# Kernel tuning notes

Measured on AMD Instinct MI355X. Metric: run time of the kernel, lower is better.

Reference implementation:

```python
import math
import jax, jax.numpy as jnp
import numpy as np

D_MODEL = 1024
NUM_HEADS = 16
D_HEAD = D_MODEL // NUM_HEADS  # 64
K_S = 32  # sparse top-k keys kept per query
B, N = 2, 2048


def setup_inputs() -> dict:
    key = jax.random.key(0)
    ks = jax.random.split(key, 9)
    s = 1.0 / math.sqrt(D_MODEL)
    return {
        "x": jax.random.normal(ks[0], (B, N, D_MODEL), dtype=jnp.float32),
        "Wq": jax.random.normal(ks[1], (D_MODEL, D_MODEL), dtype=jnp.float32) * s,
        "bq": jnp.zeros((D_MODEL,), dtype=jnp.float32),
        "Wk": jax.random.normal(ks[2], (D_MODEL, D_MODEL), dtype=jnp.float32) * s,
        "bk": jnp.zeros((D_MODEL,), dtype=jnp.float32),
        "Wv": jax.random.normal(ks[3], (D_MODEL, D_MODEL), dtype=jnp.float32) * s,
        "bv": jnp.zeros((D_MODEL,), dtype=jnp.float32),
        "Wo": jax.random.normal(ks[4], (D_MODEL, D_MODEL), dtype=jnp.float32) * s,
        "bo": jnp.zeros((D_MODEL,), dtype=jnp.float32),
    }


def _attn(x, Wq, bq, Wk, bk, Wv, bv, Wo, bo):
    b, n, _ = x.shape
    # projections (torch Linear: y = x W^T + b)
    q = (x @ Wq.T + bq).reshape(b, n, NUM_HEADS, D_HEAD).transpose(0, 2, 1, 3)
    k = (x @ Wk.T + bk).reshape(b, n, NUM_HEADS, D_HEAD).transpose(0, 2, 1, 3)
    v = (x @ Wv.T + bv).reshape(b, n, NUM_HEADS, D_HEAD).transpose(0, 2, 1, 3)
    # full scores [b, H, n, n]
    scores = jnp.einsum("bhqd,bhkd->bhqk", q, k) / math.sqrt(D_HEAD)
    # causal mask (triu above diagonal -> -inf)
    causal = jnp.triu(jnp.ones((n, n), dtype=bool), k=1)
    neg_inf = jnp.array(-jnp.inf, dtype=scores.dtype)
    scores = jnp.where(causal, neg_inf, scores)
    # sparse top-k: keep only K_S largest scores per query row
    vals, idx = jax.lax.top_k(scores, K_S)
    masked = jnp.full_like(scores, -jnp.inf)
    masked = jnp.put_along_axis(masked, idx, vals, axis=-1, inplace=False)
    attn = jax.nn.softmax(masked, axis=-1)  # dropout p=0.0 -> identity
    out = jnp.einsum("bhqk,bhkd->bhqd", attn, v)
    out = out.transpose(0, 2, 1, 3).reshape(b, n, D_MODEL)
    y = out @ Wo.T + bo
    return y, attn.mean(axis=1)


def reference(x, Wq, bq, Wk, bk, Wv, bv, Wo, bo):
    return _attn(x, Wq, bq, Wk, bk, Wv, bv, Wo, bo)
```

## Files before the change

kernel.cpp:

```cpp
#include <hip/hip_runtime.h>
#include <hip/hip_bf16.h>
#include <math.h>

#define BATCH   2
#define NTOK    2048
#define DMODEL  1024
#define HEADS   16
#define DHEAD   64
#define KSEL    32
#define MROWS   (BATCH * NTOK)
#define NBLK8   (NTOK / 8)

typedef short     bf16x8 __attribute__((ext_vector_type(8)));
typedef float     f32x4  __attribute__((ext_vector_type(4)));
typedef unsigned short ushort_t;
typedef unsigned long long u64;

#define GLOAD_LDS16(g, l) \
    __builtin_amdgcn_global_load_lds((const __attribute__((address_space(1))) void*)(g), \
                                     (__attribute__((address_space(3))) void*)(l), 16, 0, 0)

__device__ __forceinline__ ushort_t f2bf(float f) {
    unsigned u = __float_as_uint(f);
    unsigned r = (u + 0x7FFFu + ((u >> 16) & 1u)) >> 16;
    return (ushort_t)r;
}
__device__ __forceinline__ float bf2f(ushort_t h) {
    return __uint_as_float(((unsigned)h) << 16);
}

__global__ __launch_bounds__(256) void conv_split(const float* __restrict__ in,
                                                  ushort_t* __restrict__ hi,
                                                  ushort_t* __restrict__ lo, int n)
{
    const int i = (blockIdx.x * 256 + threadIdx.x) * 4;
    if (i + 3 < n) {
        const float4 v = *(const float4*)(in + i);
        ushort4 ph, pl;
        ph.x = f2bf(v.x); pl.x = f2bf(v.x - bf2f(ph.x));
        ph.y = f2bf(v.y); pl.y = f2bf(v.y - bf2f(ph.y));
        ph.z = f2bf(v.z); pl.z = f2bf(v.z - bf2f(ph.z));
        ph.w = f2bf(v.w); pl.w = f2bf(v.w - bf2f(ph.w));
        *(ushort4*)(hi + i) = ph;
        *(ushort4*)(lo + i) = pl;
    }
}

__global__ __launch_bounds__(256) void zero_fill(float* __restrict__ p, int n4)
{
    const int i = blockIdx.x * 256 + threadIdx.x;
    if (i < n4) ((float4*)p)[i] = (float4){0.f, 0.f, 0.f, 0.f};
}

__device__ __forceinline__ unsigned mono_key(float f) {
    const unsigned u = __float_as_uint(f);
    return (u ^ (unsigned)(((int)u >> 31) | 0x80000000)) + 1u;
}
__device__ __forceinline__ float unmono(unsigned m) {
    const unsigned u = m - 1u;
    return __uint_as_float(u ^ (unsigned)(((int)(~u) >> 31) | 0x80000000));
}

__global__ __launch_bounds__(256) void gemm_split_mfma(const ushort_t* __restrict__ Ahi,
                                                       const ushort_t* __restrict__ Alo,
                                                       const ushort_t* __restrict__ Bhi,
                                                       const ushort_t* __restrict__ Blo,
                                                       const float* __restrict__ bias,
                                                       float* __restrict__ out,
                                                       ushort_t* __restrict__ oh,
                                                       ushort_t* __restrict__ om,
                                                       ushort_t* __restrict__ ol,
                                                       int mode)
{
    __shared__ ushort_t AbufH[128 * 32];
    __shared__ ushort_t AbufL[128 * 32];
    __shared__ ushort_t BbufH[64 * 32];
    __shared__ ushort_t BbufL[64 * 32];

    const int tid  = threadIdx.x;
    const int wave = tid >> 6;
    const int lane = tid & 63;
    const int m0 = blockIdx.x * 128;
    const int n0 = blockIdx.y * 64;

    f32x4 acc[2][4];
#pragma unroll
    for (int i = 0; i < 2; ++i)
#pragma unroll
        for (int j = 0; j < 4; ++j) acc[i][j] = (f32x4){0.f, 0.f, 0.f, 0.f};

    const int ar0 = tid >> 2;
    const int ar1 = 64 + (tid >> 2);
    const int ak  = (tid & 3) << 3;
    const int br  = tid >> 2;

    const int fr = lane & 15;
    const int fk = (lane >> 4) << 3;

    for (int k0 = 0; k0 < DMODEL; k0 += 32) {
        __syncthreads();
        const size_t aoff0 = (size_t)(m0 + ar0) * DMODEL + k0 + ak;
        const size_t aoff1 = (size_t)(m0 + ar1) * DMODEL + k0 + ak;
        const size_t boff  = (size_t)(n0 + br) * DMODEL + k0 + ak;
        GLOAD_LDS16(Ahi + aoff0, AbufH + (size_t)tid * 8);
        GLOAD_LDS16(Ahi + aoff1, AbufH + (size_t)(256 + tid) * 8);
        GLOAD_LDS16(Alo + aoff0, AbufL + (size_t)tid * 8);
        GLOAD_LDS16(Alo + aoff1, AbufL + (size_t)(256 + tid) * 8);
        GLOAD_LDS16(Bhi + boff, BbufH + (size_t)tid * 8);
        GLOAD_LDS16(Blo + boff, BbufL + (size_t)tid * 8);
        __syncthreads();

        bf16x8 afh[2], afl[2], bfh[4], bfl[4];
#pragma unroll
        for (int mi = 0; mi < 2; ++mi) {
            const int ro = (wave * 32 + mi * 16 + fr) * 32 + fk;
            afh[mi] = *(const bf16x8*)(AbufH + ro);
            afl[mi] = *(const bf16x8*)(AbufL + ro);
        }
#pragma unroll
        for (int ni = 0; ni < 4; ++ni) {
            const int ro = (ni * 16 + fr) * 32 + fk;
            bfh[ni] = *(const bf16x8*)(BbufH + ro);
            bfl[ni] = *(const bf16x8*)(BbufL + ro);
        }

#pragma unroll
        for (int mi = 0; mi < 2; ++mi)
#pragma unroll
            for (int ni = 0; ni < 4; ++ni) {
                acc[mi][ni] = __builtin_amdgcn_mfma_f32_16x16x32_bf16(afh[mi], bfl[ni], acc[mi][ni], 0, 0, 0);
                acc[mi][ni] = __builtin_amdgcn_mfma_f32_16x16x32_bf16(afl[mi], bfh[ni], acc[mi][ni], 0, 0, 0);
                acc[mi][ni] = __builtin_amdgcn_mfma_f32_16x16x32_bf16(afh[mi], bfh[ni], acc[mi][ni], 0, 0, 0);
            }
    }

#pragma unroll
    for (int ni = 0; ni < 4; ++ni) {
        const int o = n0 + ni * 16 + (lane & 15);
        const float bv = bias[o];
#pragma unroll
        for (int mi = 0; mi < 2; ++mi) {
#pragma unroll
            for (int reg = 0; reg < 4; ++reg) {
                const int m = m0 + wave * 32 + mi * 16 + ((lane >> 4) << 2) + reg;
                const float v = acc[mi][ni][reg] + bv;
                if (mode == 0) {
                    out[(size_t)m * DMODEL + o] = v;
                } else {
                    const int bb = m >> 11;
                    const int n  = m & 2047;
                    const int hd = o >> 6;
                    const int d  = o & 63;
                    const size_t off = (((size_t)(bb * HEADS + hd)) * NTOK + n) * DHEAD + d;
                    if (mode == 1) {
                        out[off] = v;
                    } else {
                        const ushort_t h1 = f2bf(v);
                        const float r1 = v - bf2f(h1);
                        const ushort_t m1 = f2bf(r1);
                        const ushort_t l1 = f2bf(r1 - bf2f(m1));
                        oh[off] = h1; om[off] = m1; ol[off] = l1;
                    }
                }
            }
        }
    }
}

__global__ __launch_bounds__(256) void score_mfma(const ushort_t* __restrict__ Qh,
                                                  const ushort_t* __restrict__ Qm,
                                                  const ushort_t* __restrict__ Ql,
                                                  const ushort_t* __restrict__ Kh,
                                                  const ushort_t* __restrict__ Km,
                                                  const ushort_t* __restrict__ Kl,
                                                  unsigned* __restrict__ S,
                                                  unsigned* __restrict__ Smax,
                                                  int q0, int QC)
{
    const int kt = blockIdx.x;
    const int qt = blockIdx.y;
    const int bh = blockIdx.z;
    const int qbase = q0 + qt * 128;
    if (kt * 64 > qbase + 127) return;

    __shared__ ushort_t QhB[128 * 32], QmB[128 * 32], QlB[128 * 32];
    __shared__ ushort_t KhB[64 * 32],  KmB[64 * 32],  KlB[64 * 32];

    const int tid  = threadIdx.x;
    const int wave = tid >> 6;
    const int lane = tid & 63;

    const size_t qgbase = ((size_t)bh * NTOK + qbase) * DHEAD;
    const size_t kgbase = ((size_t)bh * NTOK + kt * 64) * DHEAD;

    f32x4 acc[2][4];
#pragma unroll
    for (int i = 0; i < 2; ++i)
#pragma unroll
        for (int j = 0; j < 4; ++j) acc[i][j] = (f32x4){0.f, 0.f, 0.f, 0.f};

#pragma unroll
    for (int kit = 0; kit < 2; ++kit) {
        const int koff = kit * 32;
        __syncthreads();
#pragma unroll
        for (int i = 0; i < 2; ++i) {
            const int c = i * 256 + tid;
            const int row = c >> 2;
            const int pos = (c & 3) ^ ((row >> 1) & 3);
            const size_t g = qgbase + (size_t)row * DHEAD + koff + pos * 8;
            GLOAD_LDS16(Qh + g, QhB + (size_t)c * 8);
            GLOAD_LDS16(Qm + g, QmB + (size_t)c * 8);
            GLOAD_LDS16(Ql + g, QlB + (size_t)c * 8);
        }
        {
            const int c = tid;
            const int row = c >> 2;
            const int pos = (c & 3) ^ ((row >> 1) & 3);
            const size_t g = kgbase + (size_t)row * DHEAD + koff + pos * 8;
            GLOAD_LDS16(Kh + g, KhB + (size_t)c * 8);
            GLOAD_LDS16(Km + g, KmB + (size_t)c * 8);
            GLOAD_LDS16(Kl + g, KlB + (size_t)c * 8);
        }
        __syncthreads();

        const int k8 = lane >> 4;

        bf16x8 qhf[2], qmf[2], qlf[2];
#pragma unroll
        for (int mi = 0; mi < 2; ++mi) {
            const int r = wave * 32 + mi * 16 + (lane & 15);
            const int ch = r * 4 + (k8 ^ ((r >> 1) & 3));
            qhf[mi] = *(const bf16x8*)(QhB + (size_t)ch * 8);
            qmf[mi] = *(const bf16x8*)(QmB + (size_t)ch * 8);
            qlf[mi] = *(const bf16x8*)(QlB + (size_t)ch * 8);
        }
        bf16x8 khf[4], kmf[4], klf[4];
#pragma unroll
        for (int ni = 0; ni < 4; ++ni) {
            const int r = ni * 16 + (lane & 15);
            const int ch = r * 4 + (k8 ^ ((r >> 1) & 3));
            khf[ni] = *(const bf16x8*)(KhB + (size_t)ch * 8);
            kmf[ni] = *(const bf16x8*)(KmB + (size_t)ch * 8);
            klf[ni] = *(const bf16x8*)(KlB + (size_t)ch * 8);
        }

#pragma unroll
        for (int mi = 0; mi < 2; ++mi)
#pragma unroll
            for (int ni = 0; ni < 4; ++ni) {
                acc[mi][ni] = __builtin_amdgcn_mfma_f32_16x16x32_bf16(qhf[mi], klf[ni], acc[mi][ni], 0, 0, 0);
                acc[mi][ni] = __builtin_amdgcn_mfma_f32_16x16x32_bf16(qlf[mi], khf[ni], acc[mi][ni], 0, 0, 0);
                acc[mi][ni] = __builtin_amdgcn_mfma_f32_16x16x32_bf16(qmf[mi], kmf[ni], acc[mi][ni], 0, 0, 0);
                acc[mi][ni] = __builtin_amdgcn_mfma_f32_16x16x32_bf16(qhf[mi], kmf[ni], acc[mi][ni], 0, 0, 0);
                acc[mi][ni] = __builtin_amdgcn_mfma_f32_16x16x32_bf16(qmf[mi], khf[ni], acc[mi][ni], 0, 0, 0);
                acc[mi][ni] = __builtin_amdgcn_mfma_f32_16x16x32_bf16(qhf[mi], khf[ni], acc[mi][ni], 0, 0, 0);
            }
    }

#pragma unroll
    for (int ni = 0; ni < 4; ++ni) {
        const int col = kt * 64 + ni * 16 + (lane & 15);
#pragma unroll
        for (int mi = 0; mi < 2; ++mi) {
#pragma unroll
            for (int reg = 0; reg < 4; ++reg) {
                const int mrow = wave * 32 + mi * 16 + ((lane >> 4) << 2) + reg;
                const int qlrow = qt * 128 + mrow;
                const int qglob = qbase + mrow;
                const unsigned mk = mono_key(acc[mi][ni][reg] * 0.125f);
                S[((size_t)bh * QC + qlrow) * NTOK + col] = mk;
                unsigned cm = (col <= qglob) ? mk : 0u;
                {
                    unsigned o;
                    o = __shfl_xor(cm, 1, 64); cm = (o > cm) ? o : cm;
                    o = __shfl_xor(cm, 2, 64); cm = (o > cm) ? o : cm;
                    o = __shfl_xor(cm, 4, 64); cm = (o > cm) ? o : cm;
                }
                if ((lane & 7) == 0) {
                    const int gblk = kt * 8 + ni * 2 + ((lane >> 3) & 1);
                    Smax[((size_t)bh * QC + qlrow) * NBLK8 + gblk] = cm;
                }
            }
        }
    }
}

__global__ __launch_bounds__(256) void select_v6(const unsigned* __restrict__ S,
                                                 const unsigned* __restrict__ Smax,
                                                 const float* __restrict__ V,
                                                 float* __restrict__ ctx,
                                                 float* __restrict__ attn,
                                                 int q0, int QC)
{
    __shared__ int   sBlkAll[4][KSEL];
    __shared__ int   sIdxAll[4][KSEL];
    __shared__ float sEAll[4][KSEL];

    const int lane = threadIdx.x & 63;
    const int wave = threadIdx.x >> 6;
    const int ql = blockIdx.x;
    const int b  = blockIdx.y >> 2;
    const int hg = blockIdx.y & 3;
    const int h  = hg * 4 + wave;
    const int q  = q0 + ql;
    const int L  = q + 1;
    const int nsel = (L < KSEL) ? L : KSEL;
    const int nb = (L + 7) >> 3;

    const size_t bhx = (size_t)(b * HEADS + h);
    const unsigned* Srow = S + (bhx * QC + ql) * NTOK;
    const unsigned* Mrow = Smax + (bhx * QC + ql) * NBLK8;
    const float* Vb   = V + bhx * NTOK * DHEAD;
    float* ctxRow  = ctx + (((size_t)(b * NTOK + q)) * HEADS + h) * DHEAD;
    float* attnRow = attn + ((size_t)(b * NTOK + q)) * NTOK;
    int*   sBlk = sBlkAll[wave];
    int*   sIdx = sIdxAll[wave];
    float* sE   = sEAll[wave];

    const uint4 bm4 = *(const uint4*)(Mrow + lane * 4);
    unsigned bmax[4] = {bm4.x, bm4.y, bm4.z, bm4.w};
#pragma unroll
    for (int s = 0; s < 4; ++s)
        if (lane * 4 + s >= nb) bmax[s] = 0u;

    unsigned gmax = bmax[0];
    gmax = (bmax[1] > gmax) ? bmax[1] : gmax;
    gmax = (bmax[2] > gmax) ? bmax[2] : gmax;
    gmax = (bmax[3] > gmax) ? bmax[3] : gmax;
#pragma unroll
    for (int d = 1; d < 64; d <<= 1) {
        const unsigned o = __shfl_xor(gmax, d, 64);
        gmax = (o > gmax) ? o : gmax;
    }
    const float vmax = unmono(gmax);

    unsigned selb = 0u;
    unsigned blkLo = 1u;
    int nselb;
    if (nb <= KSEL) {
        nselb = nb;
#pragma unroll
        for (int s = 0; s < 4; ++s)
            if (lane * 4 + s < nb) selb |= 1u << s;
    } else {
        nselb = KSEL;
        unsigned lo = 1u, hi = gmax >> 16;
        while (lo < hi) {
            const unsigned mid = lo + ((hi - lo + 1u) >> 1);
            const unsigned midk = mid << 16;
            int cnt = 0;
#pragma unroll
            for (int s = 0; s < 4; ++s)
                cnt += __popcll(__ballot(bmax[s] >= midk));
            if (cnt >= KSEL) lo = mid; else hi = mid - 1u;
        }
        blkLo = lo;
        const unsigned Tkb = lo << 16;
        const unsigned Gkb = Tkb | 0xFFFFu;
        int cge = 0, cgt = 0;
#pragma unroll
        for (int s = 0; s < 4; ++s) {
            cge += __popcll(__ballot(bmax[s] >= Tkb));
            cgt += __popcll(__ballot(bmax[s] > Gkb));
        }
        if (cge == KSEL) {
#pragma unroll
            for (int s = 0; s < 4; ++s)
                selb |= (bmax[s] >= Tkb) ? (1u << s) : 0u;
        } else {
            unsigned bmb = 0u;
#pragma unroll
            for (int s = 0; s < 4; ++s) {
                selb |= (bmax[s] > Gkb) ? (1u << s) : 0u;
                bmb  |= (bmax[s] >= Tkb && bmax[s] <= Gkb) ? (1u << s) : 0u;
            }
            int k_tie = KSEL - cgt;
            while (k_tie > 0) {
                u64 best = 0;
                unsigned bmm = bmb;
                while (bmm) {
                    const int s = __builtin_ctz(bmm);
                    bmm &= bmm - 1u;
                    const unsigned gblk = (unsigned)(lane * 4 + s);
                    const u64 k = ((u64)bmax[s] << 32) | (unsigned)~gblk;
                    if (k > best) best = k;
                }
                u64 bb = best;
#pragma unroll
                for (int d = 1; d < 64; d <<= 1) {
                    const u64 o = __shfl_xor(bb, d, 64);
                    bb = (o > bb) ? o : bb;
                }
                const unsigned gblk = ~(unsigned)bb;
                if (lane == (int)(gblk >> 2)) {
                    const unsigned bit = 1u << (gblk & 3u);
                    selb |= bit;
                    bmb &= ~bit;
                }
                --k_tie;
            }
        }
    }

    {
        const int cb = __popc(selb);
        int pfxb = cb;
#pragma unroll
        for (int d = 1; d < 64; d <<= 1) {
            const int t = __shfl_up(pfxb, d, 64);
            if (lane >= d) pfxb += t;
        }
        pfxb -= cb;
        unsigned mskb = selb;
        int posb = pfxb;
        while (mskb) {
            const int s = __builtin_ctz(mskb);
            mskb &= mskb - 1u;
            sBlk[posb++] = lane * 4 + s;
        }
    }
    __asm volatile("s_waitcnt lgkmcnt(0)" ::: "memory");

    const int NC = nselb * 8;
    unsigned km[4];
    int idx[4];
#pragma unroll
    for (int c = 0; c < 4; ++c) {
        const int t = c * 64 + lane;
        unsigned m = 0u;
        int j = 0;
        if (t < NC) {
            const int blk = sBlk[t >> 3];
            j = blk * 8 + (t & 7);
            if (j < L) m = Srow[j];
        }
        km[c] = m;
        idx[c] = j;
    }

    unsigned lo = blkLo, hi = gmax >> 16;
    while (lo < hi) {
        const unsigned mid = lo + ((hi - lo + 1u) >> 1);
        const unsigned midk = mid << 16;
        int cnt = 0;
#pragma unroll
        for (int c = 0; c < 4; ++c)
            cnt += __popcll(__ballot(km[c] >= midk));
        if (cnt >= nsel) lo = mid; else hi = mid - 1u;
    }
    const unsigned Tk = lo << 16;
    const unsigned Gk = Tk | 0xFFFFu;

    int cnt_ge = 0, cnt_gt = 0;
#pragma unroll
    for (int c = 0; c < 4; ++c) {
        cnt_ge += __popcll(__ballot(km[c] >= Tk));
        cnt_gt += __popcll(__ballot(km[c] > Gk));
    }

    unsigned selmask = 0u;
    if (cnt_ge == nsel) {
#pragma unroll
        for (int c = 0; c < 4; ++c)
            selmask |= (km[c] >= Tk) ? (1u << c) : 0u;
    } else {
        unsigned bmask = 0u;
#pragma unroll
        for (int c = 0; c < 4; ++c) {
            selmask |= (km[c] > Gk) ? (1u << c) : 0u;
            bmask   |= (km[c] >= Tk && km[c] <= Gk) ? (1u << c) : 0u;
        }
        int k_tie = nsel - cnt_gt;
        while (k_tie > 0) {
            u64 best = 0;
            unsigned bmm = bmask;
            while (bmm) {
                const int c = __builtin_ctz(bmm);
                bmm &= bmm - 1u;
                const int t = c * 64 + lane;
                const u64 k = ((u64)km[c] << 32) |
                              ((u64)(0xFFFFu ^ (unsigned)idx[c]) << 16) | (u64)t;
                if (k > best) best = k;
            }
            u64 bb = best;
#pragma unroll
            for (int d = 1; d < 64; d <<= 1) {
                const u64 o = __shfl_xor(bb, d, 64);
                bb = (o > bb) ? o : bb;
            }
            const unsigned tt = (unsigned)bb & 0xFFFFu;
            if (lane == (int)(tt & 63u)) {
                const unsigned bit = 1u << (tt >> 6);
                selmask |= bit;
                bmask &= ~bit;
            }
            --k_tie;
        }
    }

    const int csel = __popc(selmask);
    int pfx = csel;
#pragma unroll
    for (int d = 1; d < 64; d <<= 1) {
        const int t = __shfl_up(pfx, d, 64);
        if (lane >= d) pfx += t;
    }
    pfx -= csel;

    float esum = 0.f;
    unsigned msk = selmask;
    int pos = pfx;
    while (msk) {
        const int c = __builtin_ctz(msk);
        msk &= msk - 1u;
        const float e = __expf(unmono(km[c]) - vmax);
        esum += e;
        sIdx[pos] = idx[c];
        sE[pos] = e;
        ++pos;
    }

    float Z = esum;
#pragma unroll
    for (int d = 1; d < 64; d <<= 1) Z += __shfl_xor(Z, d, 64);
    const float rcpZ = 1.0f / Z;

    msk = selmask;
    pos = pfx;
    while (msk) {
        const int c = __builtin_ctz(msk);
        msk &= msk - 1u;
        const float w = sE[pos] * rcpZ;
        ++pos;
        atomicAdd(&attnRow[idx[c]], w * (1.0f / (float)HEADS));
    }

    float acc = 0.f;
    for (int i = 0; i < nsel; ++i) {
        const int id = sIdx[i];
        const float wi = sE[i] * rcpZ;
        acc += wi * Vb[(size_t)id * DHEAD + lane];
    }
    ctxRow[lane] = acc;
}

extern "C" void kernel_launch(void* const* d_in, const int* in_sizes, int n_in,
                              void* d_out, int out_size, void* d_ws, size_t ws_size,
                              hipStream_t stream) {
    const float* x  = (const float*)d_in[0];
    const float* Wq = (const float*)d_in[1];
    const float* bq = (const float*)d_in[2];
    const float* Wk = (const float*)d_in[3];
    const float* bk = (const float*)d_in[4];
    const float* Wv = (const float*)d_in[5];
    const float* bv = (const float*)d_in[6];
    const float* Wo = (const float*)d_in[7];
    const float* bo = (const float*)d_in[8];

    const size_t MB = 1ull << 20;
    char* wsb = (char*)d_ws;
    float*    Vws = (float*)(wsb + 0 * MB);
    float*    ctx = (float*)(wsb + 16 * MB);
    ushort_t* xhi = (ushort_t*)(wsb + 32 * MB);
    ushort_t* xlo = (ushort_t*)(wsb + 40 * MB);
    ushort_t* wqh = (ushort_t*)(wsb + 48 * MB);
    ushort_t* wql = (ushort_t*)(wsb + 50 * MB);
    ushort_t* wkh = (ushort_t*)(wsb + 52 * MB);
    ushort_t* wkl = (ushort_t*)(wsb + 54 * MB);
    ushort_t* wvh = (ushort_t*)(wsb + 56 * MB);
    ushort_t* wvl = (ushort_t*)(wsb + 58 * MB);
    ushort_t* woh = (ushort_t*)(wsb + 60 * MB);
    ushort_t* wol = (ushort_t*)(wsb + 62 * MB);
    ushort_t* Qh  = (ushort_t*)(wsb + 64 * MB);
    ushort_t* Qm  = (ushort_t*)(wsb + 72 * MB);
    ushort_t* Ql  = (ushort_t*)(wsb + 80 * MB);
    ushort_t* Kh  = (ushort_t*)(wsb + 88 * MB);
    ushort_t* Km  = (ushort_t*)(wsb + 96 * MB);
    ushort_t* Kl  = (ushort_t*)(wsb + 104 * MB);
    ushort_t* cxh = xhi;
    ushort_t* cxl = xlo;

    float* y    = (float*)d_out;
    float* attn = y + (size_t)BATCH * NTOK * DMODEL;

    const int NX = MROWS * DMODEL;
    const int NW = DMODEL * DMODEL;

    conv_split<<<NX / (256 * 4), 256, 0, stream>>>(x, xhi, xlo, NX);
    conv_split<<<NW / (256 * 4), 256, 0, stream>>>(Wq, wqh, wql, NW);
    conv_split<<<NW / (256 * 4), 256, 0, stream>>>(Wk, wkh, wkl, NW);
    conv_split<<<NW / (256 * 4), 256, 0, stream>>>(Wv, wvh, wvl, NW);
    conv_split<<<NW / (256 * 4), 256, 0, stream>>>(Wo, woh, wol, NW);

    dim3 ggrid(MROWS / 128, DMODEL / 64);
    gemm_split_mfma<<<ggrid, 256, 0, stream>>>(xhi, xlo, wqh, wql, bq, nullptr, Qh, Qm, Ql, 2);
    gemm_split_mfma<<<ggrid, 256, 0, stream>>>(xhi, xlo, wkh, wkl, bk, nullptr, Kh, Km, Kl, 2);
    gemm_split_mfma<<<ggrid, 256, 0, stream>>>(xhi, xlo, wvh, wvl, bv, Vws, nullptr, nullptr, nullptr, 1);

    const size_t base_bytes = 112 * MB;
    const size_t avail = (ws_size > base_bytes) ? ws_size - base_bytes : 0;
    int QC = 128;
    for (int cand = NTOK; cand >= 128; cand >>= 1) {
        const size_t need = (size_t)BATCH * HEADS * cand * (size_t)(NTOK + NBLK8) * sizeof(unsigned);
        if (need <= avail) { QC = cand; break; }
    }
    unsigned* Smax = (unsigned*)(wsb + base_bytes);
    unsigned* Sws  = (unsigned*)(wsb + base_bytes +
                                 (size_t)BATCH * HEADS * QC * NBLK8 * sizeof(unsigned));

    const int nattn4 = BATCH * NTOK * NTOK / 4;
    zero_fill<<<(nattn4 + 255) / 256, 256, 0, stream>>>(attn, nattn4);
    for (int q0 = 0; q0 < NTOK; q0 += QC) {
        dim3 sgrid((q0 + QC) >> 6, QC / 128, BATCH * HEADS);
        score_mfma<<<sgrid, 256, 0, stream>>>(Qh, Qm, Ql, Kh, Km, Kl, Sws, Smax, q0, QC);
        dim3 selgrid(QC, BATCH * 4);
        select_v6<<<selgrid, 256, 0, stream>>>(Sws, Smax, Vws, ctx, attn, q0, QC);
    }

    conv_split<<<NX / (256 * 4), 256, 0, stream>>>(ctx, cxh, cxl, NX);
    gemm_split_mfma<<<ggrid, 256, 0, stream>>>(cxh, cxl, woh, wol, bo, y, nullptr, nullptr, nullptr, 0);
}
```

Measured before the change: 602.5 us.

## Keep Q fragments in registers and stream 8 K tiles per score block

The score kernel now loads the 128-row Q tile once, keeps its three split-bf16 planes in registers, and loops over up to eight 64-key K tiles per block with double-buffered asynchronous LDS staging. Before, every key tile reloaded Q. The MFMA operands are swapped (K as A, Q as B), so each lane holds four consecutive key columns and writes them with a single uint4 store, which also cuts the shuffle reduction for block maxima to one step. Launch bounds request 3 blocks per CU. The trade-offs are higher register pressure and fewer blocks in the grid, which may leave the causal triangle's work unevenly spread across blocks.

Result: faster. 553.5 us (-8.1%).

```diff
diff --git a/kernel.cpp b/kernel.cpp
--- a/kernel.cpp
+++ b/kernel.cpp
@@ -10,6 +10,7 @@
 #define KSEL    32
 #define MROWS   (BATCH * NTOK)
 #define NBLK8   (NTOK / 8)
+#define TPW     8
 
 typedef short     bf16x8 __attribute__((ext_vector_type(8)));
 typedef float     f32x4  __attribute__((ext_vector_type(4)));
@@ -167,123 +168,170 @@
     }
 }
 
-__global__ __launch_bounds__(256) void score_mfma(const ushort_t* __restrict__ Qh,
-                                                  const ushort_t* __restrict__ Qm,
-                                                  const ushort_t* __restrict__ Ql,
-                                                  const ushort_t* __restrict__ Kh,
-                                                  const ushort_t* __restrict__ Km,
-                                                  const ushort_t* __restrict__ Kl,
-                                                  unsigned* __restrict__ S,
-                                                  unsigned* __restrict__ Smax,
-                                                  int q0, int QC)
+__global__ __launch_bounds__(256, 3) void score_mfma(const ushort_t* __restrict__ Qh,
+                                                     const ushort_t* __restrict__ Qm,
+                                                     const ushort_t* __restrict__ Ql,
+                                                     const ushort_t* __restrict__ Kh,
+                                                     const ushort_t* __restrict__ Km,
+                                                     const ushort_t* __restrict__ Kl,
+                                                     unsigned* __restrict__ S,
+                                                     unsigned* __restrict__ Smax,
+                                                     int q0, int QC)
 {
-    const int kt = blockIdx.x;
+    const int ks = blockIdx.x;
     const int qt = blockIdx.y;
     const int bh = blockIdx.z;
     const int qbase = q0 + qt * 128;
-    if (kt * 64 > qbase + 127) return;
-
-    __shared__ ushort_t QhB[128 * 32], QmB[128 * 32], QlB[128 * 32];
-    __shared__ ushort_t KhB[64 * 32],  KmB[64 * 32],  KlB[64 * 32];
+    const int ktmax = ((qbase + 127) >> 6) + 1;
+    const int kt0 = ks * TPW;
+    if (kt0 >= ktmax) return;
+    const int kt1 = (kt0 + TPW < ktmax) ? (kt0 + TPW) : ktmax;
+
+    __shared__ ushort_t smem[24576];
 
     const int tid  = threadIdx.x;
     const int wave = tid >> 6;
     const int lane = tid & 63;
+    const int l15  = lane & 15;
+    const int l4   = lane >> 4;
 
     const size_t qgbase = ((size_t)bh * NTOK + qbase) * DHEAD;
-    const size_t kgbase = ((size_t)bh * NTOK + kt * 64) * DHEAD;
-
-    f32x4 acc[2][4];
-#pragma unroll
-    for (int i = 0; i < 2; ++i)
-#pragma unroll
-        for (int j = 0; j < 4; ++j) acc[i][j] = (f32x4){0.f, 0.f, 0.f, 0.f};
-
-#pragma unroll
-    for (int kit = 0; kit < 2; ++kit) {
-        const int koff = kit * 32;
+
+    {
+        const ushort_t* Qp0 = Qh; const ushort_t* Qp1 = Qm; const ushort_t* Qp2 = Ql;
+#pragma unroll
+        for (int i = 0; i < 4; ++i) {
+            const int c = i * 256 + tid;
+            const int row = c >> 3;
+            const int g = (c & 7) ^ (row & 7);
+            const size_t goff = qgbase + (size_t)row * DHEAD + g * 8;
+            GLOAD_LDS16(Qp0 + goff, smem + 0 * 8192 + (size_t)c * 8);
+            GLOAD_LDS16(Qp1 + goff, smem + 1 * 8192 + (size_t)c * 8);
+            GLOAD_LDS16(Qp2 + goff, smem + 2 * 8192 + (size_t)c * 8);
+        }
+    }
+    __syncthreads();
+
+    bf16x8 qf[3][2][2];
+#pragma unroll
+    for (int p = 0; p < 3; ++p)
+#pragma unroll
+        for (int j = 0; j < 2; ++j) {
+            const int r = wave * 32 + j * 16 + l15;
+#pragma unroll
+            for (int h = 0; h < 2; ++h) {
+                const int slot = (h * 4 + l4) ^ (r & 7);
+                qf[p][j][h] = *(const bf16x8*)(smem + p * 8192 + (size_t)(r * 8 + slot) * 8);
+            }
+        }
+    __syncthreads();
+
+#define STAGE_K(bufsel, ktv) do {                                              \
+        const size_t kg_ = ((size_t)bh * NTOK + (ktv) * 64) * DHEAD;           \
+        _Pragma("unroll")                                                      \
+        for (int i_ = 0; i_ < 2; ++i_) {                                       \
+            const int c_ = i_ * 256 + tid;                                     \
+            const int row_ = c_ >> 3;                                          \
+            const int g_ = (c_ & 7) ^ (row_ & 7);                              \
+            const size_t goff_ = kg_ + (size_t)row_ * DHEAD + g_ * 8;          \
+            ushort_t* dst_ = smem + (bufsel) * 12288 + (size_t)c_ * 8;         \
+            GLOAD_LDS16(Kh + goff_, dst_ + 0 * 4096);                          \
+            GLOAD_LDS16(Km + goff_, dst_ + 1 * 4096);                          \
+            GLOAD_LDS16(Kl + goff_, dst_ + 2 * 4096);                          \
+        }                                                                      \
+    } while (0)
+
+    STAGE_K(0, kt0);
+    int cur = 0;
+
+    const size_t srowQ = (size_t)bh * QC;
+
+    for (int kt = kt0; kt < kt1; ++kt) {
         __syncthreads();
-#pragma unroll
-        for (int i = 0; i < 2; ++i) {
-            const int c = i * 256 + tid;
-            const int row = c >> 2;
-            const int pos = (c & 3) ^ ((row >> 1) & 3);
-            const size_t g = qgbase + (size_t)row * DHEAD + koff + pos * 8;
-            GLOAD_LDS16(Qh + g, QhB + (size_t)c * 8);
-            GLOAD_LDS16(Qm + g, QmB + (size_t)c * 8);
-            GLOAD_LDS16(Ql + g, QlB + (size_t)c * 8);
-        }
-        {
-            const int c = tid;
-            const int row = c >> 2;
-            const int pos = (c & 3) ^ ((row >> 1) & 3);
-            const size_t g = kgbase + (size_t)row * DHEAD + koff + pos * 8;
-            GLOAD_LDS16(Kh + g, KhB + (size_t)c * 8);
-            GLOAD_LDS16(Km + g, KmB + (size_t)c * 8);
-            GLOAD_LDS16(Kl + g, KlB + (size_t)c * 8);
-        }
-        __syncthreads();
-
-        const int k8 = lane >> 4;
-
-        bf16x8 qhf[2], qmf[2], qlf[2];
-#pragma unroll
-        for (int mi = 0; mi < 2; ++mi) {
-            const int r = wave * 32 + mi * 16 + (lane & 15);
-            const int ch = r * 4 + (k8 ^ ((r >> 1) & 3));
-            qhf[mi] = *(const bf16x8*)(QhB + (size_t)ch * 8);
-            qmf[mi] = *(const bf16x8*)(QmB + (size_t)ch * 8);
-            qlf[mi] = *(const bf16x8*)(QlB + (size_t)ch * 8);
-        }
-        bf16x8 khf[4], kmf[4], klf[4];
-#pragma unroll
-        for (int ni = 0; ni < 4; ++ni) {
-            const int r = ni * 16 + (lane & 15);
-            const int ch = r * 4 + (k8 ^ ((r >> 1) & 3));
-            khf[ni] = *(const bf16x8*)(KhB + (size_t)ch * 8);
-            kmf[ni] = *(const bf16x8*)(KmB + (size_t)ch * 8);
-            klf[ni] = *(const bf16x8*)(KlB + (size_t)ch * 8);
-        }
-
-#pragma unroll
-        for (int mi = 0; mi < 2; ++mi)
-#pragma unroll
-            for (int ni = 0; ni < 4; ++ni) {
-                acc[mi][ni] = __builtin_amdgcn_mfma_f32_16x16x32_bf16(qhf[mi], klf[ni], acc[mi][ni], 0, 0, 0);
-                acc[mi][ni] = __builtin_amdgcn_mfma_f32_16x16x32_bf16(qlf[mi], khf[ni], acc[mi][ni], 0, 0, 0);
-                acc[mi][ni] = __builtin_amdgcn_mfma_f32_16x16x32_bf16(qmf[mi], kmf[ni], acc[mi][ni], 0, 0, 0);
-                acc[mi][ni] = __builtin_amdgcn_mfma_f32_16x16x32_bf16(qhf[mi], kmf[ni], acc[mi][ni], 0, 0, 0);
-                acc[mi][ni] = __builtin_amdgcn_mfma_f32_16x16x32_bf16(qmf[mi], khf[ni], acc[mi][ni], 0, 0, 0);
-                acc[mi][ni] = __builtin_amdgcn_mfma_f32_16x16x32_bf16(qhf[mi], khf[ni], acc[mi][ni], 0, 0, 0);
-            }
-    }
-
-#pragma unroll
-    for (int ni = 0; ni < 4; ++ni) {
-        const int col = kt * 64 + ni * 16 + (lane & 15);
-#pragma unroll
-        for (int mi = 0; mi < 2; ++mi) {
-#pragma unroll
-            for (int reg = 0; reg < 4; ++reg) {
-                const int mrow = wave * 32 + mi * 16 + ((lane >> 4) << 2) + reg;
-                const int qlrow = qt * 128 + mrow;
-                const int qglob = qbase + mrow;
-                const unsigned mk = mono_key(acc[mi][ni][reg] * 0.125f);
-                S[((size_t)bh * QC + qlrow) * NTOK + col] = mk;
-                unsigned cm = (col <= qglob) ? mk : 0u;
-                {
-                    unsigned o;
-                    o = __shfl_xor(cm, 1, 64); cm = (o > cm) ? o : cm;
-                    o = __shfl_xor(cm, 2, 64); cm = (o > cm) ? o : cm;
-                    o = __shfl_xor(cm, 4, 64); cm = (o > cm) ? o : cm;
+        if (kt + 1 < kt1) STAGE_K(cur ^ 1, kt + 1);
+
+        f32x4 acc[4][2];
+#pragma unroll
+        for (int m = 0; m < 4; ++m)
+#pragma unroll
+            for (int j = 0; j < 2; ++j) acc[m][j] = (f32x4){0.f, 0.f, 0.f, 0.f};
+
+        const ushort_t* kb = smem + cur * 12288;
+#pragma unroll
+        for (int h = 0; h < 2; ++h) {
+            bf16x8 kf[4];
+#pragma unroll
+            for (int m = 0; m < 4; ++m) {
+                const int r = m * 16 + l15;
+                const int slot = (h * 4 + l4) ^ (r & 7);
+                kf[m] = *(const bf16x8*)(kb + 0 * 4096 + (size_t)(r * 8 + slot) * 8);
+            }
+#pragma unroll
+            for (int m = 0; m < 4; ++m)
+#pragma unroll
+                for (int j = 0; j < 2; ++j) {
+                    acc[m][j] = __builtin_amdgcn_mfma_f32_16x16x32_bf16(kf[m], qf[2][j][h], acc[m][j], 0, 0, 0);
+                    acc[m][j] = __builtin_amdgcn_mfma_f32_16x16x32_bf16(kf[m], qf[1][j][h], acc[m][j], 0, 0, 0);
+                    acc[m][j] = __builtin_amdgcn_mfma_f32_16x16x32_bf16(kf[m], qf[0][j][h], acc[m][j], 0, 0, 0);
                 }
-                if ((lane & 7) == 0) {
-                    const int gblk = kt * 8 + ni * 2 + ((lane >> 3) & 1);
-                    Smax[((size_t)bh * QC + qlrow) * NBLK8 + gblk] = cm;
+#pragma unroll
+            for (int m = 0; m < 4; ++m) {
+                const int r = m * 16 + l15;
+                const int slot = (h * 4 + l4) ^ (r & 7);
+                kf[m] = *(const bf16x8*)(kb + 1 * 4096 + (size_t)(r * 8 + slot) * 8);
+            }
+#pragma unroll
+            for (int m = 0; m < 4; ++m)
+#pragma unroll
+                for (int j = 0; j < 2; ++j) {
+                    acc[m][j] = __builtin_amdgcn_mfma_f32_16x16x32_bf16(kf[m], qf[1][j][h], acc[m][j], 0, 0, 0);
+                    acc[m][j] = __builtin_amdgcn_mfma_f32_16x16x32_bf16(kf[m], qf[0][j][h], acc[m][j], 0, 0, 0);
                 }
-            }
-        }
-    }
+#pragma unroll
+            for (int m = 0; m < 4; ++m) {
+                const int r = m * 16 + l15;
+                const int slot = (h * 4 + l4) ^ (r & 7);
+                kf[m] = *(const bf16x8*)(kb + 2 * 4096 + (size_t)(r * 8 + slot) * 8);
+            }
+#pragma unroll
+            for (int m = 0; m < 4; ++m)
+#pragma unroll
+                for (int j = 0; j < 2; ++j)
+                    acc[m][j] = __builtin_amdgcn_mfma_f32_16x16x32_bf16(kf[m], qf[0][j][h], acc[m][j], 0, 0, 0);
+        }
+
+#pragma unroll
+        for (int j = 0; j < 2; ++j) {
+            const int qrow  = wave * 32 + j * 16 + l15;
+            const int qlrow = qt * 128 + qrow;
+            const int qglob = qbase + qrow;
+            const size_t srow = (srowQ + qlrow) * NTOK;
+            const size_t mrow = (srowQ + qlrow) * NBLK8;
+#pragma unroll
+            for (int m = 0; m < 4; ++m) {
+                const int kcol0 = kt * 64 + m * 16 + (l4 << 2);
+                uint4 kv;
+                kv.x = mono_key(acc[m][j][0] * 0.125f);
+                kv.y = mono_key(acc[m][j][1] * 0.125f);
+                kv.z = mono_key(acc[m][j][2] * 0.125f);
+                kv.w = mono_key(acc[m][j][3] * 0.125f);
+                *(uint4*)(S + srow + kcol0) = kv;
+                unsigned cm = (kcol0     <= qglob) ? kv.x : 0u;
+                unsigned t;
+                t = (kcol0 + 1 <= qglob) ? kv.y : 0u; cm = (t > cm) ? t : cm;
+                t = (kcol0 + 2 <= qglob) ? kv.z : 0u; cm = (t > cm) ? t : cm;
+                t = (kcol0 + 3 <= qglob) ? kv.w : 0u; cm = (t > cm) ? t : cm;
+                const unsigned o = __shfl_xor(cm, 16, 64);
+                cm = (o > cm) ? o : cm;
+                if ((lane & 16) == 0) {
+                    const int gblk = kt * 8 + m * 2 + (lane >> 5);
+                    Smax[mrow + gblk] = cm;
+                }
+            }
+        }
+        cur ^= 1;
+    }
+#undef STAGE_K
 }
 
 __global__ __launch_bounds__(256) void select_v6(const unsigned* __restrict__ S,
@@ -612,7 +660,8 @@
     const int nattn4 = BATCH * NTOK * NTOK / 4;
     zero_fill<<<(nattn4 + 255) / 256, 256, 0, stream>>>(attn, nattn4);
     for (int q0 = 0; q0 < NTOK; q0 += QC) {
-        dim3 sgrid((q0 + QC) >> 6, QC / 128, BATCH * HEADS);
+        const int ktm = (q0 + QC) >> 6;
+        dim3 sgrid((ktm + TPW - 1) / TPW, QC / 128, BATCH * HEADS);
         score_mfma<<<sgrid, 256, 0, stream>>>(Qh, Qm, Ql, Kh, Km, Kl, Sws, Smax, q0, QC);
         dim3 selgrid(QC, BATCH * 4);
         select_v6<<<selgrid, 256, 0, stream>>>(Sws, Smax, Vws, ctx, attn, q0, QC);
```
